# Optimization experiments

Hardware: AMD Instinct MI355X
Metric: run time of the kernel (lower is better)

Reference implementation:

```python
import jax, jax.numpy as jnp
import numpy as np

D_MODEL = 1024
NUM_HEADS = 8
KEY_DIM = 768      # int(1024*0.75)
VALUE_DIM = 1536   # int(1024*1.5)
HQK = KEY_DIM // NUM_HEADS    # 96
HV = VALUE_DIM // NUM_HEADS   # 192
D_CONV = 4
CHUNK = 64
B, L = 2, 4096


def silu(x):
    return x * jax.nn.sigmoid(x)


def causal_dwconv(x, w):
    # x: (B, L, C), w: (C, K) depthwise kernel; causal (left pad K-1), matches
    # torch Conv1d(padding=K-1) followed by [:, :L] slice.
    K = w.shape[1]
    Lx = x.shape[1]
    xp = jnp.pad(x, ((0, 0), (K - 1, 0), (0, 0)))
    out = xp[:, 0:Lx, :] * w[:, 0]
    for j in range(1, K):
        out = out + xp[:, j:j + Lx, :] * w[:, j]
    return out


def chunk_gated_delta_rule(q, k, v, beta, g, c):
    # q,k: (B,H,L,Dk) L2-normalized; v: (B,H,L,Dv); beta,g: (B,H,L)
    b, h, l, dk = q.shape
    dv = v.shape[-1]
    n = l // c  # L chosen as multiple of chunk size
    q = q * (dk ** -0.5)
    v = v * beta[..., None]
    kb = k * beta[..., None]
    rs = lambda x: x.reshape(b, h, n, c, x.shape[-1])
    q, k, v, kb = rs(q), rs(k), rs(v), rs(kb)
    dec = jnp.cumsum(g.reshape(b, h, n, c), axis=-1)        # (b,h,n,c)
    Lmask = jnp.exp(jnp.minimum(dec[..., :, None] - dec[..., None, :], 0.0))  # (b,h,n,c,c)
    tri_incl = jnp.triu(jnp.ones((c, c), bool))   # upper incl diag -> zeroed
    striu = jnp.triu(jnp.ones((c, c), bool), 1)   # strict upper
    I = jnp.eye(c, dtype=jnp.float32)
    KK = jnp.einsum('bhncd,bhnmd->bhncm', kb, k)  # k_beta @ k^T
    M1 = I + jnp.where(tri_incl, 0.0, KK * Lmask)
    M2 = I + jnp.where(tri_incl, 0.0, KK)
    Ib = jnp.broadcast_to(I, M1.shape)
    solve = lambda M: jax.lax.linalg.triangular_solve(
        M, Ib, left_side=True, lower=True, unit_diagonal=True)
    u_ = solve(M1) @ v       # k_cumsum (= u)
    kcd = solve(M2) @ kb     # k_cumdecay

    def step(S, xs):
        qi, ki, ui, kci, Lmi, di = xs
        ed = jnp.exp(di)[..., None]                 # (b,h,c,1)
        attn = jnp.where(striu, 0.0, jnp.einsum('bhcd,bhmd->bhcm', qi, ki) * Lmi)
        v_new = ui - jnp.einsum('bhcd,bhde->bhce', kci * ed, S)
        oi = jnp.einsum('bhcd,bhde->bhce', qi * ed, S) + attn @ v_new
        dl = di[..., -1]                            # (b,h)
        S = S * jnp.exp(dl)[..., None, None] + jnp.einsum(
            'bhcd,bhce->bhde', ki * jnp.exp(dl[..., None] - di)[..., None], v_new)
        return S, oi

    xs = tuple(jnp.moveaxis(t, 2, 0) for t in (q, k, u_, kcd, Lmask, dec))
    S0 = jnp.zeros((b, h, dk, dv), jnp.float32)
    _, o = jax.lax.scan(step, S0, xs)               # o: (n,b,h,c,dv)
    return jnp.moveaxis(o, 0, 2).reshape(b, h, l, dv)


def setup_inputs() -> dict:
    key = jax.random.key(0)
    ks = jax.random.split(key, 16)
    w = lambda k, shape: (jax.random.normal(k, shape, jnp.float32) * 0.02)
    dt = jnp.exp(jax.random.uniform(ks[10], (NUM_HEADS,)) *
                 (np.log(0.1) - np.log(0.001)) + np.log(0.001))
    dt = jnp.clip(dt, 0.0001, None)
    inv_dt = dt + jnp.log(-jnp.expm1(-dt))
    return {
        'u': jax.random.normal(ks[0], (B, L, D_MODEL), jnp.float32),
        'Wq': w(ks[1], (D_MODEL, KEY_DIM)),
        'Wk': w(ks[2], (D_MODEL, KEY_DIM)),
        'Wv': w(ks[3], (D_MODEL, VALUE_DIM)),
        'Wg': w(ks[4], (D_MODEL, VALUE_DIM)),
        'Wo': w(ks[5], (VALUE_DIM, D_MODEL)),
        'Wgk': w(ks[6], (D_MODEL, NUM_HEADS)),
        'Wb': w(ks[7], (D_MODEL, NUM_HEADS)),
        'b_b': jnp.zeros((NUM_HEADS,), jnp.float32),
        'A_log': jnp.log(jax.random.uniform(ks[8], (NUM_HEADS,), minval=0.001, maxval=16.0)),
        'dt_bias': inv_dt.astype(jnp.float32),
        'conv_q': w(ks[11], (KEY_DIM, D_CONV)) * 10.0,
        'conv_k': w(ks[12], (KEY_DIM, D_CONV)) * 10.0,
        'conv_v': w(ks[13], (VALUE_DIM, D_CONV)) * 10.0,
        'norm_w': jnp.ones((HV,), jnp.float32),
    }


def reference(u, Wq, Wk, Wv, Wg, Wo, Wgk, Wb, b_b, A_log, dt_bias,
              conv_q, conv_k, conv_v, norm_w):
    b, l, _ = u.shape
    q = silu(causal_dwconv(u @ Wq, conv_q))
    k = silu(causal_dwconv(u @ Wk, conv_k))
    v = silu(causal_dwconv(u @ Wv, conv_v))
    gk = u @ Wgk                                    # (B,L,H)
    gk = -jnp.exp(A_log) * jax.nn.softplus(gk + dt_bias)
    gk = gk.transpose(0, 2, 1)                      # (B,H,L)
    beta = jax.nn.sigmoid(u @ Wb + b_b).transpose(0, 2, 1)
    to_bhl = lambda x, d: x.reshape(b, l, NUM_HEADS, d).transpose(0, 2, 1, 3)
    q = to_bhl(q, HQK)
    k = to_bhl(k, HQK)
    v = to_bhl(v, HV)
    l2n = lambda x: x / jnp.maximum(jnp.linalg.norm(x, axis=-1, keepdims=True), 1e-12)
    q, k = l2n(q), l2n(k)
    o = chunk_gated_delta_rule(q, k, v, beta, gk, CHUNK)  # (B,H,L,HV)
    o = o.transpose(0, 2, 1, 3)                     # (B,L,H,HV)
    g = (u @ Wg).reshape(b, l, NUM_HEADS, HV)
    # RMSNormGated, norm_before_gate=True: norm(x)*weight*silu(g)
    on = o * jax.lax.rsqrt(jnp.mean(o * o, axis=-1, keepdims=True) + 1e-5) * norm_w
    on = on * silu(g)
    return on.reshape(b, l, VALUE_DIM) @ Wo
```

## Files before the change

### kernel.cpp

```cpp
#include <hip/hip_runtime.h>

using u16 = unsigned short;
using u32 = unsigned int;
typedef __bf16 bf16x8 __attribute__((ext_vector_type(8)));
typedef u16    u16x8  __attribute__((ext_vector_type(8)));
typedef float  f32x4  __attribute__((ext_vector_type(4)));
typedef float  f32x2  __attribute__((ext_vector_type(2)));
typedef u32    u32x4  __attribute__((ext_vector_type(4)));
typedef u32    u32x2  __attribute__((ext_vector_type(2)));

__device__ __forceinline__ float bf2f(u16 h){ u32 u = ((u32)h)<<16; float f; __builtin_memcpy(&f,&u,4); return f; }
__device__ __forceinline__ u16 f2bf(float f){ u32 u; __builtin_memcpy(&u,&f,4); u32 r = (u + 0x7FFFu + ((u>>16)&1u))>>16; return (u16)r; }
__device__ __forceinline__ float bflo(u32 w){ return bf2f((u16)(w & 0xFFFFu)); }
__device__ __forceinline__ float bfhiw(u32 w){ return bf2f((u16)(w >> 16)); }
__device__ __forceinline__ float sigx(float x){ float e = __expf(-fabsf(x)); float p = 1.f/(1.f+e); return (x>=0.f) ? p : 1.f-p; }

#define BAR_LGKM() asm volatile("s_waitcnt lgkmcnt(0)\n\ts_barrier" ::: "memory")

__device__ __forceinline__ float ldsc(const void* p, size_t i, bool f32){
  return f32 ? ((const float*)p)[i] : bf2f(((const u16*)p)[i]);
}
__device__ __forceinline__ u32x4 ld8bf(const void* p, size_t i, bool f32){
  if (!f32) return *(const u32x4*)((const u16*)p + i);
  const f32x4* q = (const f32x4*)((const float*)p + i);
  f32x4 a = q[0], b = q[1];
  u32x4 r;
  r.x = (u32)f2bf(a.x) | ((u32)f2bf(a.y)<<16);
  r.y = (u32)f2bf(a.z) | ((u32)f2bf(a.w)<<16);
  r.z = (u32)f2bf(b.x) | ((u32)f2bf(b.y)<<16);
  r.w = (u32)f2bf(b.z) | ((u32)f2bf(b.w)<<16);
  return r;
}
__device__ __forceinline__ void ld4w(const void* p, size_t i, bool f32,
                                     float& w0, float& w1, float& w2, float& w3){
  if (f32){ f32x4 v = *(const f32x4*)((const float*)p + i); w0=v.x; w1=v.y; w2=v.z; w3=v.w; }
  else { u32x2 v = *(const u32x2*)((const u16*)p + i); w0=bflo(v.x); w1=bfhiw(v.x); w2=bflo(v.y); w3=bfhiw(v.y); }
}


__global__ void detect_kernel(const u16* __restrict__ probe, int* __restrict__ flag){
  int t = threadIdx.x;
  int bad = 0;
  for (int i=t; i<1024; i+=64){
    u16 h = probe[i];
    int e = (h>>7)&0xFF;
    if (e >= 0xC0) bad = 1;
  }
  unsigned long long anyb = __ballot(bad);
  if (t==0) *flag = (anyb != 0ull) ? 1 : 0;
}

__global__ void transpose5(const void* __restrict__ Wq, const void* __restrict__ Wk,
                           const void* __restrict__ Wv, const void* __restrict__ Wg,
                           const void* __restrict__ Wo, const void* __restrict__ U,
                           u16* __restrict__ WqT, u16* __restrict__ WkT, u16* __restrict__ WvT,
                           u16* __restrict__ WgT, u16* __restrict__ WoT, u16* __restrict__ ubf,
                           const int* __restrict__ flagp){
  const bool f32 = (*flagp != 0);
  const int bid = blockIdx.x;
  const int t = threadIdx.x;
  if (bid >= 6144){
    size_t base = ((size_t)(bid-6144)*256 + t) * 16;
    u32x4 a = ld8bf(U, base, f32);
    u32x4 b = ld8bf(U, base+8, f32);
    *(u32x4*)(ubf + base)     = a;
    *(u32x4*)(ubf + base + 8) = b;
    return;
  }
  const void* in; u16* out; int C; int local;
  int R;
  if (bid < 768){ in=Wq; out=WqT; R=1024; C=768;  local=bid; }
  else if (bid < 1536){ in=Wk; out=WkT; R=1024; C=768;  local=bid-768; }
  else if (bid < 3072){ in=Wv; out=WvT; R=1024; C=1536; local=bid-1536; }
  else if (bid < 4608){ in=Wg; out=WgT; R=1024; C=1536; local=bid-3072; }
  else { in=Wo; out=WoT; R=1536; C=1024; local=bid-4608; }
  const int nCx = C>>5;
  const int c0 = (local % nCx)*32, r0 = (local / nCx)*32;
  __shared__ u16 tile[32][33];
  int tx = t & 31, ty = t >> 5;
  #pragma unroll
  for (int j=0;j<4;j++){
    int r = r0 + ty + j*8;
    size_t g = (size_t)r*C + c0 + tx;
    tile[ty+j*8][tx] = f32 ? f2bf(((const float*)in)[g]) : ((const u16*)in)[g];
  }
  __syncthreads();
  #pragma unroll
  for (int j=0;j<4;j++){ int c = c0 + ty + j*8; out[(size_t)c*R + r0 + tx] = tile[tx][ty+j*8]; }
}

__global__ __launch_bounds__(256,2) void gemm_bt(const void* __restrict__ A, const u16* __restrict__ Bt,
                                                 void* __restrict__ C, int M, int N, int K,
                                                 const int* __restrict__ flagp, int a_ext, int c_ext,
                                                 int sanitize){
  __shared__ __align__(16) u16 As[128*32];
  __shared__ __align__(16) u16 Bs[128*32];
  const int fl = *flagp;
  const bool af32 = a_ext && fl;
  const bool cf32 = c_ext && fl;
  const int t = threadIdx.x;
  const int bid = blockIdx.x;
  const int nbn = N>>7, rpx = (M>>7)>>3;
  const int x2 = bid & 7, s = bid >> 3;
  const int bm = (x2*rpx + s/nbn)*128;
  const int bn = (s % nbn)*128;
  const int wave = t>>6, lane = t&63, quad = lane>>4, l16 = lane&15;
  const int wm = (wave>>1)*64, wn = (wave&1)*64;
  f32x4 acc[4][4] = {};
  const int row0 = t>>2, kp = (t&3)*8;
  const size_t iA0 = (size_t)(bm+row0)*K + kp;
  const size_t iA1 = iA0 + (size_t)64*K;
  const u16* pB0 = Bt + (size_t)(bn+row0)*K + kp;
  const u16* pB1 = pB0 + (size_t)64*K;
  u32x4 ra0 = ld8bf(A, iA0, af32);
  u32x4 ra1 = ld8bf(A, iA1, af32);
  u32x4 rb0 = *(const u32x4*)pB0;
  u32x4 rb1 = *(const u32x4*)pB1;
  const int nk = K>>5;
  for (int kt=0; kt<nk; ++kt){
    __syncthreads();
    ((u32x4*)As)[t]     = ra0;
    ((u32x4*)As)[t+256] = ra1;
    ((u32x4*)Bs)[t]     = rb0;
    ((u32x4*)Bs)[t+256] = rb1;
    __syncthreads();
    if (kt+1 < nk){
      int o = (kt+1)*32;
      ra0 = ld8bf(A, iA0 + o, af32); ra1 = ld8bf(A, iA1 + o, af32);
      rb0 = *(const u32x4*)(pB0 + o); rb1 = *(const u32x4*)(pB1 + o);
    }
    bf16x8 af[4], bfv[4];
    #pragma unroll
    for (int i=0;i<4;i++){
      af[i]  = *(const bf16x8*)&As[(wm + i*16 + l16)*32 + quad*8];
      bfv[i] = *(const bf16x8*)&Bs[(wn + i*16 + l16)*32 + quad*8];
    }
    #pragma unroll
    for (int i=0;i<4;i++)
      #pragma unroll
      for (int j=0;j<4;j++)
        acc[i][j] = __builtin_amdgcn_mfma_f32_16x16x32_bf16(af[i], bfv[j], acc[i][j], 0,0,0);
  }
  #pragma unroll
  for (int i=0;i<4;i++)
    #pragma unroll
    for (int j=0;j<4;j++)
      #pragma unroll
      for (int r2=0;r2<4;r2++){
        int m = bm + wm + i*16 + quad*4 + r2;
        int n = bn + wn + j*16 + l16;
        float v = acc[i][j][r2];
        if (sanitize && !(v==v && v<1e30f && v>-1e30f)) v = 0.f;
        if (cf32) ((float*)C)[(size_t)m*N + n] = v;
        else      ((u16*)C)[(size_t)m*N + n] = f2bf(v);
      }
}

__global__ __launch_bounds__(256,2) void gemm_qkv(const u16* __restrict__ A,
                                                  const u16* __restrict__ BtQ, const u16* __restrict__ BtK,
                                                  const u16* __restrict__ BtV,
                                                  u16* __restrict__ Cq, u16* __restrict__ Ck, u16* __restrict__ Cv){
  __shared__ __align__(16) u16 As[128*32];
  __shared__ __align__(16) u16 Bs[128*32];
  const int t = threadIdx.x;
  const int bid = blockIdx.x;
  const int x2 = bid & 7, s = bid >> 3;
  const int bm = (x2*8 + s/24)*128;
  const int cgrp = s % 24;
  const u16* Bt; u16* C; int N, bn;
  if (cgrp < 6){ Bt=BtQ; C=Cq; N=768; bn=cgrp*128; }
  else if (cgrp < 12){ Bt=BtK; C=Ck; N=768; bn=(cgrp-6)*128; }
  else { Bt=BtV; C=Cv; N=1536; bn=(cgrp-12)*128; }
  const int K = 1024;
  const int wave = t>>6, lane = t&63, quad = lane>>4, l16 = lane&15;
  const int wm = (wave>>1)*64, wn = (wave&1)*64;
  f32x4 acc[4][4] = {};
  const int row0 = t>>2, kp = (t&3)*8;
  const u16* pA0 = A + (size_t)(bm+row0)*K + kp;
  const u16* pA1 = pA0 + (size_t)64*K;
  const u16* pB0 = Bt + (size_t)(bn+row0)*K + kp;
  const u16* pB1 = pB0 + (size_t)64*K;
  u32x4 ra0 = *(const u32x4*)pA0;
  u32x4 ra1 = *(const u32x4*)pA1;
  u32x4 rb0 = *(const u32x4*)pB0;
  u32x4 rb1 = *(const u32x4*)pB1;
  for (int kt=0; kt<32; ++kt){
    __syncthreads();
    ((u32x4*)As)[t]     = ra0;
    ((u32x4*)As)[t+256] = ra1;
    ((u32x4*)Bs)[t]     = rb0;
    ((u32x4*)Bs)[t+256] = rb1;
    __syncthreads();
    if (kt+1 < 32){
      int o = (kt+1)*32;
      ra0 = *(const u32x4*)(pA0 + o); ra1 = *(const u32x4*)(pA1 + o);
      rb0 = *(const u32x4*)(pB0 + o); rb1 = *(const u32x4*)(pB1 + o);
    }
    bf16x8 af[4], bfv[4];
    #pragma unroll
    for (int i=0;i<4;i++){
      af[i]  = *(const bf16x8*)&As[(wm + i*16 + l16)*32 + quad*8];
      bfv[i] = *(const bf16x8*)&Bs[(wn + i*16 + l16)*32 + quad*8];
    }
    #pragma unroll
    for (int i=0;i<4;i++)
      #pragma unroll
      for (int j=0;j<4;j++)
        acc[i][j] = __builtin_amdgcn_mfma_f32_16x16x32_bf16(af[i], bfv[j], acc[i][j], 0,0,0);
  }
  #pragma unroll
  for (int i=0;i<4;i++)
    #pragma unroll
    for (int j=0;j<4;j++)
      #pragma unroll
      for (int r2=0;r2<4;r2++){
        int m = bm + wm + i*16 + quad*4 + r2;
        int n = bn + wn + j*16 + l16;
        C[(size_t)m*N + n] = f2bf(acc[i][j][r2]);
      }
}

__global__ __launch_bounds__(256) void prep_kernel(
    const void* __restrict__ u, const void* __restrict__ Wgk, const void* __restrict__ Wb,
    const void* __restrict__ b_b, const void* __restrict__ A_log, const void* __restrict__ dt_b,
    const u16* __restrict__ qraw, const u16* __restrict__ kraw, const u16* __restrict__ vraw,
    const void* __restrict__ cq, const void* __restrict__ ck, const void* __restrict__ cv,
    float* __restrict__ gk, float* __restrict__ beta,
    u16* __restrict__ qn, u16* __restrict__ kn, u16* __restrict__ vb,
    const int* __restrict__ flagp){
  const bool f32 = (*flagp != 0);
  const int bl = blockIdx.x;
  const int b = bl>>12, l = bl&4095;
  const int t = threadIdx.x;
  __shared__ float s[768];
  __shared__ float red[4][16];
  __shared__ float nrm[8];
  __shared__ float bS2[8];

  {
    float accg[8] = {0,0,0,0,0,0,0,0};
    float accb[8] = {0,0,0,0,0,0,0,0};
    for (int d=t; d<1024; d+=256){
      float uv = ldsc(u, (size_t)bl*1024 + d, f32);
      u32x4 wg = ld8bf(Wgk, (size_t)d*8, f32);
      u32x4 wb = ld8bf(Wb,  (size_t)d*8, f32);
      accg[0] += uv*bflo(wg.x); accg[1] += uv*bfhiw(wg.x);
      accg[2] += uv*bflo(wg.y); accg[3] += uv*bfhiw(wg.y);
      accg[4] += uv*bflo(wg.z); accg[5] += uv*bfhiw(wg.z);
      accg[6] += uv*bflo(wg.w); accg[7] += uv*bfhiw(wg.w);
      accb[0] += uv*bflo(wb.x); accb[1] += uv*bfhiw(wb.x);
      accb[2] += uv*bflo(wb.y); accb[3] += uv*bfhiw(wb.y);
      accb[4] += uv*bflo(wb.z); accb[5] += uv*bfhiw(wb.z);
      accb[6] += uv*bflo(wb.w); accb[7] += uv*bfhiw(wb.w);
    }
    #pragma unroll
    for (int h=0;h<8;h++){
      #pragma unroll
      for (int off=32; off>=1; off>>=1){
        accg[h] += __shfl_down(accg[h], off);
        accb[h] += __shfl_down(accb[h], off);
      }
    }
    int wv = t>>6, lane = t&63;
    if (lane==0){
      #pragma unroll
      for (int h=0;h<8;h++){ red[wv][h]=accg[h]; red[wv][8+h]=accb[h]; }
    }
    __syncthreads();
    if (t<16){
      float sum = red[0][t]+red[1][t]+red[2][t]+red[3][t];
      if (t<8){
        int h=t;
        float x = sum + ldsc(dt_b, h, f32);
        float sp = (x>20.f) ? x : log1pf(__expf(x));
        gk[(size_t)(b*8+h)*4096 + l] = -__expf(ldsc(A_log, h, f32)) * sp;
      } else {
        int h=t-8;
        float x = sum + ldsc(b_b, h, f32);
        float bv = sigx(x);
        beta[(size_t)(b*8+h)*4096 + l] = bv;
        bS2[h] = bv;
      }
    }
  }
  __syncthreads();

  const int base = b*4096;
  for (int c=t; c<768; c+=256){
    float w0,w1,w2,w3; ld4w(cq, (size_t)c*4, f32, w0,w1,w2,w3);
    float acc = 0.f;
    if (l>=3) acc += bf2f(qraw[(size_t)(base+l-3)*768 + c])*w0;
    if (l>=2) acc += bf2f(qraw[(size_t)(base+l-2)*768 + c])*w1;
    if (l>=1) acc += bf2f(qraw[(size_t)(base+l-1)*768 + c])*w2;
    acc += bf2f(qraw[(size_t)(base+l)*768 + c])*w3;
    s[c] = acc*sigx(acc);
  }
  __syncthreads();
  {
    int h = t>>5, l32 = t&31;
    float p = 0.f;
    for (int i=l32; i<96; i+=32){ float x = s[h*96+i]; p += x*x; }
    p += __shfl_down(p,16,32); p += __shfl_down(p,8,32); p += __shfl_down(p,4,32);
    p += __shfl_down(p,2,32);  p += __shfl_down(p,1,32);
    if (l32==0) nrm[h] = fmaxf(sqrtf(p), 1e-12f);
  }
  __syncthreads();
  for (int c=t; c<768; c+=256){
    int hh = c/96; int d = c - hh*96;
    float v = s[c]/nrm[hh]*0.10206207261596575f;
    qn[((size_t)(b*8+hh)*4096 + l)*96 + d] = f2bf(v);
  }
  __syncthreads();
  for (int c=t; c<768; c+=256){
    float w0,w1,w2,w3; ld4w(ck, (size_t)c*4, f32, w0,w1,w2,w3);
    float acc = 0.f;
    if (l>=3) acc += bf2f(kraw[(size_t)(base+l-3)*768 + c])*w0;
    if (l>=2) acc += bf2f(kraw[(size_t)(base+l-2)*768 + c])*w1;
    if (l>=1) acc += bf2f(kraw[(size_t)(base+l-1)*768 + c])*w2;
    acc += bf2f(kraw[(size_t)(base+l)*768 + c])*w3;
    s[c] = acc*sigx(acc);
  }
  __syncthreads();
  {
    int h = t>>5, l32 = t&31;
    float p = 0.f;
    for (int i=l32; i<96; i+=32){ float x = s[h*96+i]; p += x*x; }
    p += __shfl_down(p,16,32); p += __shfl_down(p,8,32); p += __shfl_down(p,4,32);
    p += __shfl_down(p,2,32);  p += __shfl_down(p,1,32);
    if (l32==0) nrm[h] = fmaxf(sqrtf(p), 1e-12f);
  }
  __syncthreads();
  for (int c=t; c<768; c+=256){
    int hh = c/96; int d = c - hh*96;
    float v = s[c]/nrm[hh]*1.0f;
    kn[((size_t)(b*8+hh)*4096 + l)*96 + d] = f2bf(v);
  }
  for (int c=t; c<1536; c+=256){
    float w0,w1,w2,w3; ld4w(cv, (size_t)c*4, f32, w0,w1,w2,w3);
    float acc = 0.f;
    if (l>=3) acc += bf2f(vraw[(size_t)(base+l-3)*1536 + c])*w0;
    if (l>=2) acc += bf2f(vraw[(size_t)(base+l-2)*1536 + c])*w1;
    if (l>=1) acc += bf2f(vraw[(size_t)(base+l-1)*1536 + c])*w2;
    acc += bf2f(vraw[(size_t)(base+l)*1536 + c])*w3;
    int h = c/192; int d = c - h*192;
    vb[((size_t)(b*8+h)*4096 + l)*192 + d] = f2bf(acc*sigx(acc)*bS2[h]);
  }
}

__global__ __launch_bounds__(320,2) void chunkprep_kernel(
    const u16* __restrict__ qn, u16* __restrict__ knw, const u16* __restrict__ vb,
    const float* __restrict__ beta, const float* __restrict__ gk,
    u16* __restrict__ attn, u16* __restrict__ kcd, u16* __restrict__ uA,
    float* __restrict__ edG, float* __restrict__ aG){
  __shared__ __align__(16) u16 kS[64*104];
  __shared__ __align__(16) u16 qS[64*104];
  __shared__ float M1[64*64];
  __shared__ float M2[64*64];
  __shared__ float bS[64], dS[64], wS2[64];
  const int t = threadIdx.x;
  const int bhn = blockIdx.x;
  const size_t rowb = (size_t)bhn*64;
  const int w = t>>6, l = t&63, l16 = l&15, quad = l>>4;

  #pragma unroll
  for (int j=0;j<3;j++){
    int v = t + 320*j;
    if (v < 768){
      int rr = v/12, c8 = v - rr*12;
      size_t g = (rowb+rr)*96 + c8*8;
      *(u32x4*)&kS[rr*104 + c8*8] = *(const u32x4*)(knw + g);
      *(u32x4*)&qS[rr*104 + c8*8] = *(const u32x4*)(qn + g);
    }
  }
  if (t<64){
    bS[t] = beta[rowb+t];
    float g = gk[rowb+t];
    #pragma unroll
    for (int off=1; off<64; off<<=1){
      float xx = __shfl_up(g, off);
      if (t >= off) g += xx;
    }
    dS[t] = g;
    float dl = __shfl(g, 63);
    edG[rowb+t] = __expf(g);
    wS2[t] = __expf(dl - g);
    if (t==0) aG[bhn] = __expf(dl);
  }
  __syncthreads();

  for (int idx=t; idx<6144; idx+=320){
    int d = idx>>6, ll = idx&63;
    knw[(size_t)bhn*6144 + idx] = f2bf(bf2f(kS[ll*104 + d])*wS2[ll]);
  }

  float x[64];
  const int mode0 = (t<192) ? 0 : 1;
  const int c0 = (t<192) ? t : (t-192);
  const bool active = (t < 288);
  if (active){
    if (mode0==0){
      #pragma unroll
      for (int i=0;i<64;i++) x[i] = bf2f(vb[(rowb+i)*192 + c0]);
    } else {
      #pragma unroll
      for (int i=0;i<64;i++) x[i] = bS[i]*bf2f(kS[i*104 + c0]);
    }
  }

  if (t < 256){
    bf16x8 qA[3], kA[3];
    #pragma unroll
    for (int ks=0;ks<3;ks++){
      qA[ks] = *(const bf16x8*)&qS[(w*16+l16)*104 + ks*32 + quad*8];
      kA[ks] = *(const bf16x8*)&kS[(w*16+l16)*104 + ks*32 + quad*8];
    }
    const size_t ab = (size_t)bhn*4096;
    #pragma unroll
    for (int nt=0;nt<4;nt++){
      f32x4 aQ = {0.f,0.f,0.f,0.f}, aK = {0.f,0.f,0.f,0.f};
      #pragma unroll
      for (int ks=0;ks<3;ks++){
        bf16x8 Bf = *(const bf16x8*)&kS[(nt*16+l16)*104 + ks*32 + quad*8];
        aQ = __builtin_amdgcn_mfma_f32_16x16x32_bf16(qA[ks], Bf, aQ,0,0,0);
        aK = __builtin_amdgcn_mfma_f32_16x16x32_bf16(kA[ks], Bf, aK,0,0,0);
      }
      #pragma unroll
      for (int r=0;r<4;r++){
        int row = w*16 + quad*4 + r;
        int col = nt*16 + l16;
        float lm = __expf(fminf(dS[row]-dS[col], 0.f));
        attn[ab + row*64 + col] = (col<=row) ? f2bf(aQ[r]*lm) : (u16)0;
        if (col<row){
          float kkb = aK[r]*bS[row];
          M2[row*64+col] = kkb;
          M1[row*64+col] = kkb*lm;
        }
      }
    }
  }
  __syncthreads();

  if (active){
    const float* Mb = (mode0==0) ? M1 : M2;
    #pragma unroll
    for (int i=1;i<64;i++){
      float acc = x[i];
      #pragma unroll
      for (int m=0;m<i;m++) acc -= Mb[i*64+m]*x[m];
      x[i] = acc;
    }
    if (mode0==0){
      #pragma unroll
      for (int i=0;i<64;i++) uA[(rowb+i)*192 + c0] = f2bf(x[i]);
    } else {
      #pragma unroll
      for (int i=0;i<64;i++) kcd[(rowb+i)*96 + c0] = f2bf(x[i]);
    }
  }
}

__global__ __launch_bounds__(256,1) void scan_glin_kernel(
    const u16* __restrict__ qn, const u16* __restrict__ kTw, const u16* __restrict__ kcd,
    const u16* __restrict__ attn, const u16* __restrict__ uA,
    const float* __restrict__ edG, const float* __restrict__ aG,
    u16* __restrict__ o,
    const u16* __restrict__ Ag, const u16* __restrict__ Btg,
    u16* __restrict__ Cg0, u16* __restrict__ Cg1, u16* __restrict__ Cg2, u16* __restrict__ Cg3){
  __shared__ __align__(16) char smem[16640];
  const int bid = blockIdx.x;
  const int t = threadIdx.x;

  if (bid >= 192){
    u16* As = (u16*)smem;
    u16* Bs = (u16*)(smem + 8192);
    const int j = bid - 192;
    const int x2 = j & 7, s = j >> 3;
    const int bm = (x2*8 + s/12)*128;
    const int bn = (s % 12)*128;
    const int wave = t>>6, lane = t&63, quad = lane>>4, l16 = lane&15;
    const int wm = (wave>>1)*64, wn = (wave&1)*64;
    f32x4 acc[4][4] = {};
    const int row0 = t>>2, kp = (t&3)*8;
    const u16* pA0 = Ag + (size_t)(bm+row0)*1024 + kp;
    const u16* pA1 = pA0 + (size_t)64*1024;
    const u16* pB0 = Btg + (size_t)(bn+row0)*1024 + kp;
    const u16* pB1 = pB0 + (size_t)64*1024;
    u32x4 ra0 = *(const u32x4*)pA0;
    u32x4 ra1 = *(const u32x4*)pA1;
    u32x4 rb0 = *(const u32x4*)pB0;
    u32x4 rb1 = *(const u32x4*)pB1;
    for (int kt=0; kt<32; ++kt){
      __syncthreads();
      ((u32x4*)As)[t]     = ra0;
      ((u32x4*)As)[t+256] = ra1;
      ((u32x4*)Bs)[t]     = rb0;
      ((u32x4*)Bs)[t+256] = rb1;
      __syncthreads();
      if (kt+1 < 32){
        int o2 = (kt+1)*32;
        ra0 = *(const u32x4*)(pA0 + o2); ra1 = *(const u32x4*)(pA1 + o2);
        rb0 = *(const u32x4*)(pB0 + o2); rb1 = *(const u32x4*)(pB1 + o2);
      }
      bf16x8 af[4], bfv[4];
      #pragma unroll
      for (int i=0;i<4;i++){
        af[i]  = *(const bf16x8*)&As[(wm + i*16 + l16)*32 + quad*8];
        bfv[i] = *(const bf16x8*)&Bs[(wn + i*16 + l16)*32 + quad*8];
      }
      #pragma unroll
      for (int i=0;i<4;i++)
        #pragma unroll
        for (int j2=0;j2<4;j2++)
          acc[i][j2] = __builtin_amdgcn_mfma_f32_16x16x32_bf16(af[i], bfv[j2], acc[i][j2], 0,0,0);
    }
    u16* Cp; int mo;
    if (bm < 5376){ Cp = Cg0; mo = bm; }
    else if (bm < 6656){ Cp = Cg1; mo = bm - 5376; }
    else if (bm < 7680){ Cp = Cg2; mo = bm - 6656; }
    else { Cp = Cg3; mo = bm - 7680; }
    #pragma unroll
    for (int i=0;i<4;i++)
      #pragma unroll
      for (int j2=0;j2<4;j2++)
        #pragma unroll
        for (int r2=0;r2<4;r2++){
          int m = mo + wm + i*16 + quad*4 + r2;
          int n = bn + wn + j2*16 + l16;
          Cp[(size_t)m*1536 + n] = f2bf(acc[i][j2][r2]);
        }
    return;
  }

  __builtin_amdgcn_s_setprio(1);
  const int bh = bid % 16, eg = bid / 16;
  const int e0 = eg*16;
  const int w = t>>6, l = t&63, l16 = l&15, quad = l>>4;

  u16* vnewT = (u16*)smem;
  u16* Sbf   = (u16*)(smem + 2304);

  for (int i=t; i<16*104; i+=256) Sbf[i] = 0;

  size_t rowb = (size_t)bh*4096;
  size_t ab   = (size_t)bh*64*4096;

  u32x4 kcdF[3], qF[3], attF[2]; u16 uF[4];
  u32x4 kuC[2][2], kuN[2][2];
  auto pfAB = [&](size_t rowbN){
    #pragma unroll
    for (int ks=0; ks<3; ks++){
      size_t gg = (rowbN + w*16 + l16)*96 + ks*32 + quad*8;
      kcdF[ks] = *(const u32x4*)(kcd + gg);
      qF[ks]   = *(const u32x4*)(qn + gg);
    }
  };
  auto pfATT = [&](size_t abN){
    #pragma unroll
    for (int ks=0; ks<2; ks++)
      attF[ks] = *(const u32x4*)(attn + abN + (w*16 + l16)*64 + ks*32 + quad*8);
  };
  auto pfU = [&](size_t rowbN){
    #pragma unroll
    for (int r=0;r<4;r++)
      uF[r] = uA[(rowbN + w*16 + quad*4 + r)*192 + e0 + l16];
  };
  auto pfKU = [&](size_t chunkIdx, u32x4 (&dst)[2][2]){
    #pragma unroll
    for (int i=0;i<2;i++){
      int tid = w + 4*i;
      if (tid < 6){
        size_t base = chunkIdx*6144 + (size_t)(tid*16 + l16)*64 + quad*8;
        dst[i][0] = *(const u32x4*)(kTw + base);
        dst[i][1] = *(const u32x4*)(kTw + base + 32);
      }
    }
  };

  pfAB(rowb); pfU(rowb); pfATT(ab);
  pfKU(rowb>>6, kuC);
  f32x4 edC = *(const f32x4*)&edG[rowb + w*16 + quad*4];
  float aexpC = aG[rowb>>6];
  __syncthreads();
  f32x4 Sreg[2] = {};

  for (int n=0;n<64;n++){
    const size_t rowbN = rowb + 64;
    const size_t abN = ab + 4096;
    f32x4 edN = {0.f,0.f,0.f,0.f};
    float aexpN = 0.f;
    if (n<63){
      pfKU(rowbN>>6, kuN);
      edN = *(const f32x4*)&edG[rowbN + w*16 + quad*4];
      aexpN = aG[rowbN>>6];
    }
    f32x4 accA = {0.f,0.f,0.f,0.f}, accQ = {0.f,0.f,0.f,0.f};
    #pragma unroll
    for (int ks=0;ks<3;ks++){
      bf16x8 Bf = *(const bf16x8*)&Sbf[l16*104 + ks*32 + quad*8];
      accA = __builtin_amdgcn_mfma_f32_16x16x32_bf16(*(const bf16x8*)&kcdF[ks], Bf, accA,0,0,0);
      accQ = __builtin_amdgcn_mfma_f32_16x16x32_bf16(*(const bf16x8*)&qF[ks],  Bf, accQ,0,0,0);
    }
    #pragma unroll
    for (int r=0;r<4;r++){
      float vn = bf2f(uF[r]) - edC[r]*accA[r];
      vnewT[l16*72 + (w*16+quad*4+r)] = f2bf(vn);
      accQ[r] *= edC[r];
    }
    if (n<63){ pfAB(rowbN); pfU(rowbN); }
    BAR_LGKM();
    #pragma unroll
    for (int ks=0;ks<2;ks++){
      bf16x8 Bv = *(const bf16x8*)&vnewT[l16*72 + ks*32 + quad*8];
      accQ = __builtin_amdgcn_mfma_f32_16x16x32_bf16(*(const bf16x8*)&attF[ks], Bv, accQ,0,0,0);
    }
    #pragma unroll
    for (int r=0;r<4;r++)
      o[(rowb + w*16 + quad*4 + r)*192 + e0 + l16] = f2bf(accQ[r]);
    if (n<63) pfATT(abN);
    #pragma unroll
    for (int i=0;i<2;i++){
      int tid = w + 4*i;
      if (tid < 6){
        int mt = tid;
        f32x4 acc = (f32x4){0.f,0.f,0.f,0.f};
        #pragma unroll
        for (int ks=0;ks<2;ks++){
          bf16x8 Bv = *(const bf16x8*)&vnewT[l16*72 + ks*32 + quad*8];
          acc = __builtin_amdgcn_mfma_f32_16x16x32_bf16(*(const bf16x8*)&kuC[i][ks], Bv, acc,0,0,0);
        }
        f32x4 ns;
        ns.x = Sreg[i].x*aexpC + acc.x;
        ns.y = Sreg[i].y*aexpC + acc.y;
        ns.z = Sreg[i].z*aexpC + acc.z;
        ns.w = Sreg[i].w*aexpC + acc.w;
        Sreg[i] = ns;
        u32x2 pv;
        pv.x = (u32)f2bf(ns.x) | ((u32)f2bf(ns.y)<<16);
        pv.y = (u32)f2bf(ns.z) | ((u32)f2bf(ns.w)<<16);
        *(u32x2*)&Sbf[l16*104 + mt*16 + quad*4] = pv;
      }
    }
    BAR_LGKM();
    rowb = rowbN; ab = abN;
    edC = edN; aexpC = aexpN;
    kuC[0][0]=kuN[0][0]; kuC[0][1]=kuN[0][1]; kuC[1][0]=kuN[1][0]; kuC[1][1]=kuN[1][1];
  }
}

__global__ __launch_bounds__(192) void epilogue_kernel(const u16* __restrict__ o,
                                                       const u16* __restrict__ g0, const u16* __restrict__ g1,
                                                       const u16* __restrict__ g2, const u16* __restrict__ g3,
                                                       const void* __restrict__ nw, u16* __restrict__ on,
                                                       const int* __restrict__ flagp){
  const bool f32 = (*flagp != 0);
  const int bl = blockIdx.x; const int h = blockIdx.y; const int d = threadIdx.x;
  const int b = bl>>12, l = bl&4095;
  float x = bf2f(o[((size_t)(b*8+h)*4096 + l)*192 + d]);
  float p = x*x;
  p += __shfl_down(p,32); p += __shfl_down(p,16); p += __shfl_down(p,8);
  p += __shfl_down(p,4);  p += __shfl_down(p,2);  p += __shfl_down(p,1);
  __shared__ float red[3];
  int wv = d>>6;
  if ((d&63)==0) red[wv] = p;
  __syncthreads();
  float ss = red[0]+red[1]+red[2];
  float rs = rsqrtf(ss/192.f + 1e-5f);
  const u16* gp; int bo;
  if (bl < 5376){ gp = g0; bo = bl; }
  else if (bl < 6656){ gp = g1; bo = bl - 5376; }
  else if (bl < 7680){ gp = g2; bo = bl - 6656; }
  else { gp = g3; bo = bl - 7680; }
  float g = bf2f(gp[(size_t)bo*1536 + h*192 + d]);
  float val = x*rs*ldsc(nw, d, f32) * g*sigx(g);
  on[(size_t)bl*1536 + h*192 + d] = f2bf(val);
}

extern "C" void kernel_launch(void* const* d_in, const int* in_sizes, int n_in,
                              void* d_out, int out_size, void* d_ws, size_t ws_size,
                              hipStream_t stream){
  (void)in_sizes; (void)n_in; (void)out_size; (void)ws_size;
  const void* u     = d_in[0];
  const void* Wq    = d_in[1];
  const void* Wk    = d_in[2];
  const void* Wv    = d_in[3];
  const void* Wg    = d_in[4];
  const void* Wo    = d_in[5];
  const void* Wgk   = d_in[6];
  const void* Wb    = d_in[7];
  const void* b_b   = d_in[8];
  const void* A_log = d_in[9];
  const void* dt_b  = d_in[10];
  const void* cq    = d_in[11];
  const void* ck    = d_in[12];
  const void* cv    = d_in[13];
  const void* nw    = d_in[14];

  char* w = (char*)d_ws;
  size_t off = 0;
  auto take = [&](size_t bytes)->char*{
    char* p = w + off;
    off += (bytes + 255) & ~(size_t)255;
    return p;
  };
  int* flag = (int*)take(256);
  u16* WqT  = (u16*)take((size_t)768*1024*2);
  u16* WkT  = (u16*)take((size_t)768*1024*2);
  u16* WvT  = (u16*)take((size_t)1536*1024*2);
  u16* WgT  = (u16*)take((size_t)1536*1024*2);
  u16* WoT  = (u16*)take((size_t)1024*1536*2);
  u16* qraw = (u16*)take((size_t)8192*768*2);
  u16* kraw = (u16*)take((size_t)8192*768*2);
  u16* vraw = (u16*)take((size_t)8192*1536*2);
  u16* qn   = (u16*)take((size_t)8192*768*2);
  u16* kn   = (u16*)take((size_t)8192*768*2);
  u16* vb   = (u16*)take((size_t)8192*1536*2);
  u16* ubf  = (u16*)take((size_t)8192*1024*2);
  float* gkA   = (float*)WqT;
  float* betaA = gkA + 65536;
  float* edG   = betaA + 65536;
  float* wGA   = edG + 65536;
  float* aGA   = wGA + 65536;
  u16* attnA = qraw;
  u16* kcdA  = kraw;
  u16* uuA   = vraw;
  u16* oA    = vb;
  u16* onA   = vraw;
  u16* glin0 = (u16*)d_out;
  u16* glin1 = attnA + (size_t)1024*64*64;
  u16* glin2 = WvT;
  u16* glin3 = WkT;

  detect_kernel<<<1,64,0,stream>>>((const u16*)u, flag);
  transpose5<<<8192,256,0,stream>>>(Wq, Wk, Wv, Wg, Wo, u,
                                    WqT, WkT, WvT, WgT, WoT, ubf, flag);
  gemm_qkv<<<1536,256,0,stream>>>(ubf, WqT, WkT, WvT, qraw, kraw, vraw);
  prep_kernel<<<8192,256,0,stream>>>(u, Wgk, Wb, b_b, A_log, dt_b,
                                     qraw, kraw, vraw, cq, ck, cv,
                                     gkA, betaA, qn, kn, vb, flag);
  chunkprep_kernel<<<1024,320,0,stream>>>(qn, kn, vb, betaA, gkA, attnA, kcdA, uuA,
                                          edG, aGA);
  scan_glin_kernel<<<960,256,0,stream>>>(qn, kn , kcdA, attnA, uuA, edG, aGA, oA,
                                         ubf, WgT, glin0, glin1, glin2, glin3);
  epilogue_kernel<<<dim3(8192,8),192,0,stream>>>(oA, glin0, glin1, glin2, glin3, nw, onA, flag);
  gemm_bt<<<512,256,0,stream>>>(onA, WoT, d_out, 8192, 1024, 1536, flag, 0, 1, 1);
}
```

Measured before the change: 574.2 us.

## Vectorize prep and epilogue kernels with 8-wide bf16 loads and role-split threads

The prep kernel now runs 384 threads, each handling 8 channels of q, k or v. Each thread uses 128-bit loads for the conv inputs and weights, and the q/k L2 norms are computed in one merged pass. This removes the shared-memory staging and the several serial barrier phases. The epilogue kernel moves from one block per (position, head) with scalar elements to one block per position, where each thread handles 8 contiguous elements with vector loads and stores. This cuts block count, instruction count and memory transactions, at the cost of more registers per thread and less parallelism per block.

```diff
diff --git a/kernel.cpp b/kernel.cpp
--- a/kernel.cpp
+++ b/kernel.cpp
@@ -31,10 +31,9 @@
   r.w = (u32)f2bf(b.z) | ((u32)f2bf(b.w)<<16);
   return r;
 }
-__device__ __forceinline__ void ld4w(const void* p, size_t i, bool f32,
-                                     float& w0, float& w1, float& w2, float& w3){
-  if (f32){ f32x4 v = *(const f32x4*)((const float*)p + i); w0=v.x; w1=v.y; w2=v.z; w3=v.w; }
-  else { u32x2 v = *(const u32x2*)((const u16*)p + i); w0=bflo(v.x); w1=bfhiw(v.x); w2=bflo(v.y); w3=bfhiw(v.y); }
+__device__ __forceinline__ void unpack8(u32x4 v, float* f){
+  f[0]=bflo(v.x); f[1]=bfhiw(v.x); f[2]=bflo(v.y); f[3]=bfhiw(v.y);
+  f[4]=bflo(v.z); f[5]=bfhiw(v.z); f[6]=bflo(v.w); f[7]=bfhiw(v.w);
 }
 
 
@@ -220,7 +219,7 @@
       }
 }
 
-__global__ __launch_bounds__(256) void prep_kernel(
+__global__ __launch_bounds__(384) void prep_kernel(
     const void* __restrict__ u, const void* __restrict__ Wgk, const void* __restrict__ Wb,
     const void* __restrict__ b_b, const void* __restrict__ A_log, const void* __restrict__ dt_b,
     const u16* __restrict__ qraw, const u16* __restrict__ kraw, const u16* __restrict__ vraw,
@@ -232,12 +231,12 @@
   const int bl = blockIdx.x;
   const int b = bl>>12, l = bl&4095;
   const int t = threadIdx.x;
-  __shared__ float s[768];
   __shared__ float red[4][16];
-  __shared__ float nrm[8];
+  __shared__ float sqP[96], skP[96];
+  __shared__ float nrmq[8], nrmk[8];
   __shared__ float bS2[8];
 
-  {
+  if (t < 256){
     float accg[8] = {0,0,0,0,0,0,0,0};
     float accb[8] = {0,0,0,0,0,0,0,0};
     for (int d=t; d<1024; d+=256){
@@ -266,84 +265,107 @@
       #pragma unroll
       for (int h=0;h<8;h++){ red[wv][h]=accg[h]; red[wv][8+h]=accb[h]; }
     }
-    __syncthreads();
-    if (t<16){
-      float sum = red[0][t]+red[1][t]+red[2][t]+red[3][t];
-      if (t<8){
-        int h=t;
-        float x = sum + ldsc(dt_b, h, f32);
-        float sp = (x>20.f) ? x : log1pf(__expf(x));
-        gk[(size_t)(b*8+h)*4096 + l] = -__expf(ldsc(A_log, h, f32)) * sp;
-      } else {
-        int h=t-8;
-        float x = sum + ldsc(b_b, h, f32);
-        float bv = sigx(x);
-        beta[(size_t)(b*8+h)*4096 + l] = bv;
-        bS2[h] = bv;
-      }
+  }
+  __syncthreads();
+  if (t<16){
+    float sum = red[0][t]+red[1][t]+red[2][t]+red[3][t];
+    if (t<8){
+      int h=t;
+      float x = sum + ldsc(dt_b, h, f32);
+      float sp = (x>20.f) ? x : log1pf(__expf(x));
+      gk[(size_t)(b*8+h)*4096 + l] = -__expf(ldsc(A_log, h, f32)) * sp;
+    } else {
+      int h=t-8;
+      float x = sum + ldsc(b_b, h, f32);
+      float bv = sigx(x);
+      beta[(size_t)(b*8+h)*4096 + l] = bv;
+      bS2[h] = bv;
     }
   }
   __syncthreads();
 
   const int base = b*4096;
-  for (int c=t; c<768; c+=256){
-    float w0,w1,w2,w3; ld4w(cq, (size_t)c*4, f32, w0,w1,w2,w3);
-    float acc = 0.f;
-    if (l>=3) acc += bf2f(qraw[(size_t)(base+l-3)*768 + c])*w0;
-    if (l>=2) acc += bf2f(qraw[(size_t)(base+l-2)*768 + c])*w1;
-    if (l>=1) acc += bf2f(qraw[(size_t)(base+l-1)*768 + c])*w2;
-    acc += bf2f(qraw[(size_t)(base+l)*768 + c])*w3;
-    s[c] = acc*sigx(acc);
-  }
-  __syncthreads();
-  {
-    int h = t>>5, l32 = t&31;
-    float p = 0.f;
-    for (int i=l32; i<96; i+=32){ float x = s[h*96+i]; p += x*x; }
-    p += __shfl_down(p,16,32); p += __shfl_down(p,8,32); p += __shfl_down(p,4,32);
-    p += __shfl_down(p,2,32);  p += __shfl_down(p,1,32);
-    if (l32==0) nrm[h] = fmaxf(sqrtf(p), 1e-12f);
-  }
-  __syncthreads();
-  for (int c=t; c<768; c+=256){
-    int hh = c/96; int d = c - hh*96;
-    float v = s[c]/nrm[hh]*0.10206207261596575f;
-    qn[((size_t)(b*8+hh)*4096 + l)*96 + d] = f2bf(v);
-  }
-  __syncthreads();
-  for (int c=t; c<768; c+=256){
-    float w0,w1,w2,w3; ld4w(ck, (size_t)c*4, f32, w0,w1,w2,w3);
-    float acc = 0.f;
-    if (l>=3) acc += bf2f(kraw[(size_t)(base+l-3)*768 + c])*w0;
-    if (l>=2) acc += bf2f(kraw[(size_t)(base+l-2)*768 + c])*w1;
-    if (l>=1) acc += bf2f(kraw[(size_t)(base+l-1)*768 + c])*w2;
-    acc += bf2f(kraw[(size_t)(base+l)*768 + c])*w3;
-    s[c] = acc*sigx(acc);
-  }
-  __syncthreads();
-  {
-    int h = t>>5, l32 = t&31;
-    float p = 0.f;
-    for (int i=l32; i<96; i+=32){ float x = s[h*96+i]; p += x*x; }
-    p += __shfl_down(p,16,32); p += __shfl_down(p,8,32); p += __shfl_down(p,4,32);
-    p += __shfl_down(p,2,32);  p += __shfl_down(p,1,32);
-    if (l32==0) nrm[h] = fmaxf(sqrtf(p), 1e-12f);
-  }
-  __syncthreads();
-  for (int c=t; c<768; c+=256){
-    int hh = c/96; int d = c - hh*96;
-    float v = s[c]/nrm[hh]*1.0f;
-    kn[((size_t)(b*8+hh)*4096 + l)*96 + d] = f2bf(v);
-  }
-  for (int c=t; c<1536; c+=256){
-    float w0,w1,w2,w3; ld4w(cv, (size_t)c*4, f32, w0,w1,w2,w3);
-    float acc = 0.f;
-    if (l>=3) acc += bf2f(vraw[(size_t)(base+l-3)*1536 + c])*w0;
-    if (l>=2) acc += bf2f(vraw[(size_t)(base+l-2)*1536 + c])*w1;
-    if (l>=1) acc += bf2f(vraw[(size_t)(base+l-1)*1536 + c])*w2;
-    acc += bf2f(vraw[(size_t)(base+l)*1536 + c])*w3;
-    int h = c/192; int d = c - h*192;
-    vb[((size_t)(b*8+h)*4096 + l)*192 + d] = f2bf(acc*sigx(acc)*bS2[h]);
+  int role, c0;
+  if (t < 96){ role=0; c0=t*8; }
+  else if (t < 192){ role=1; c0=(t-96)*8; }
+  else { role=2; c0=(t-192)*8; }
+  const u16* raw = (role==0)? qraw : (role==1)? kraw : vraw;
+  const void* cw = (role==0)? cq : (role==1)? ck : cv;
+  const int C = (role==2)? 1536 : 768;
+
+  float w[8][4];
+  #pragma unroll
+  for (int g=0; g<4; g++){
+    u32x4 W = ld8bf(cw, (size_t)c0*4 + g*8, f32);
+    w[g*2+0][0]=bflo(W.x); w[g*2+0][1]=bfhiw(W.x); w[g*2+0][2]=bflo(W.y); w[g*2+0][3]=bfhiw(W.y);
+    w[g*2+1][0]=bflo(W.z); w[g*2+1][1]=bfhiw(W.z); w[g*2+1][2]=bflo(W.w); w[g*2+1][3]=bfhiw(W.w);
+  }
+  float acc[8];
+  #pragma unroll
+  for (int ch=0; ch<8; ch++) acc[ch] = 0.f;
+  #pragma unroll
+  for (int j=0;j<4;j++){
+    if (l >= 3-j){
+      u32x4 iv = *(const u32x4*)(raw + (size_t)(base+l-3+j)*C + c0);
+      float in[8]; unpack8(iv, in);
+      #pragma unroll
+      for (int ch=0;ch<8;ch++) acc[ch] += in[ch]*w[ch][j];
+    }
+  }
+  #pragma unroll
+  for (int ch=0;ch<8;ch++) acc[ch] = acc[ch]*sigx(acc[ch]);
+
+  if (role==2){
+    int h = c0/192, d0 = c0 - h*192;
+    float bv = bS2[h];
+    u32x4 pv;
+    pv.x = (u32)f2bf(acc[0]*bv) | ((u32)f2bf(acc[1]*bv)<<16);
+    pv.y = (u32)f2bf(acc[2]*bv) | ((u32)f2bf(acc[3]*bv)<<16);
+    pv.z = (u32)f2bf(acc[4]*bv) | ((u32)f2bf(acc[5]*bv)<<16);
+    pv.w = (u32)f2bf(acc[6]*bv) | ((u32)f2bf(acc[7]*bv)<<16);
+    *(u32x4*)&vb[((size_t)(b*8+h)*4096 + l)*192 + d0] = pv;
+  } else {
+    float ss = 0.f;
+    #pragma unroll
+    for (int ch=0;ch<8;ch++) ss += acc[ch]*acc[ch];
+    if (role==0) sqP[t] = ss; else skP[t-96] = ss;
+  }
+  __syncthreads();
+  if (t < 8){
+    float s = 0.f;
+    #pragma unroll
+    for (int j=0;j<12;j++) s += sqP[t*12+j];
+    nrmq[t] = fmaxf(sqrtf(s), 1e-12f);
+  } else if (t < 16){
+    int h = t-8;
+    float s = 0.f;
+    #pragma unroll
+    for (int j=0;j<12;j++) s += skP[h*12+j];
+    nrmk[h] = fmaxf(sqrtf(s), 1e-12f);
+  }
+  __syncthreads();
+  if (role==0){
+    int h = c0/96, d0 = c0 - h*96;
+    float nr = nrmq[h];
+    float v0 = acc[0]/nr*0.10206207261596575f, v1 = acc[1]/nr*0.10206207261596575f;
+    float v2 = acc[2]/nr*0.10206207261596575f, v3 = acc[3]/nr*0.10206207261596575f;
+    float v4 = acc[4]/nr*0.10206207261596575f, v5 = acc[5]/nr*0.10206207261596575f;
+    float v6 = acc[6]/nr*0.10206207261596575f, v7 = acc[7]/nr*0.10206207261596575f;
+    u32x4 pv;
+    pv.x = (u32)f2bf(v0) | ((u32)f2bf(v1)<<16);
+    pv.y = (u32)f2bf(v2) | ((u32)f2bf(v3)<<16);
+    pv.z = (u32)f2bf(v4) | ((u32)f2bf(v5)<<16);
+    pv.w = (u32)f2bf(v6) | ((u32)f2bf(v7)<<16);
+    *(u32x4*)&qn[((size_t)(b*8+h)*4096 + l)*96 + d0] = pv;
+  } else if (role==1){
+    int h = c0/96, d0 = c0 - h*96;
+    float nr = nrmk[h];
+    u32x4 pv;
+    pv.x = (u32)f2bf(acc[0]/nr*1.0f) | ((u32)f2bf(acc[1]/nr*1.0f)<<16);
+    pv.y = (u32)f2bf(acc[2]/nr*1.0f) | ((u32)f2bf(acc[3]/nr*1.0f)<<16);
+    pv.z = (u32)f2bf(acc[4]/nr*1.0f) | ((u32)f2bf(acc[5]/nr*1.0f)<<16);
+    pv.w = (u32)f2bf(acc[6]/nr*1.0f) | ((u32)f2bf(acc[7]/nr*1.0f)<<16);
+    *(u32x4*)&kn[((size_t)(b*8+h)*4096 + l)*96 + d0] = pv;
   }
 }
 
@@ -653,26 +675,45 @@
                                                        const void* __restrict__ nw, u16* __restrict__ on,
                                                        const int* __restrict__ flagp){
   const bool f32 = (*flagp != 0);
-  const int bl = blockIdx.x; const int h = blockIdx.y; const int d = threadIdx.x;
+  const int bl = blockIdx.x;
+  const int t = threadIdx.x;
   const int b = bl>>12, l = bl&4095;
-  float x = bf2f(o[((size_t)(b*8+h)*4096 + l)*192 + d]);
-  float p = x*x;
-  p += __shfl_down(p,32); p += __shfl_down(p,16); p += __shfl_down(p,8);
-  p += __shfl_down(p,4);  p += __shfl_down(p,2);  p += __shfl_down(p,1);
-  __shared__ float red[3];
-  int wv = d>>6;
-  if ((d&63)==0) red[wv] = p;
-  __syncthreads();
-  float ss = red[0]+red[1]+red[2];
-  float rs = rsqrtf(ss/192.f + 1e-5f);
+  const int h = t/24, d0 = (t - h*24)*8;
+  __shared__ float part[192];
+  __shared__ float rsS[8];
+  u32x4 ov = *(const u32x4*)&o[((size_t)(b*8+h)*4096 + l)*192 + d0];
+  float x[8]; unpack8(ov, x);
+  float ss = 0.f;
+  #pragma unroll
+  for (int ch=0;ch<8;ch++) ss += x[ch]*x[ch];
+  part[t] = ss;
+  __syncthreads();
+  if (t < 8){
+    float s = 0.f;
+    #pragma unroll
+    for (int j=0;j<24;j++) s += part[t*24+j];
+    rsS[t] = rsqrtf(s/192.f + 1e-5f);
+  }
+  __syncthreads();
+  float rs = rsS[h];
   const u16* gp; int bo;
   if (bl < 5376){ gp = g0; bo = bl; }
   else if (bl < 6656){ gp = g1; bo = bl - 5376; }
   else if (bl < 7680){ gp = g2; bo = bl - 6656; }
   else { gp = g3; bo = bl - 7680; }
-  float g = bf2f(gp[(size_t)bo*1536 + h*192 + d]);
-  float val = x*rs*ldsc(nw, d, f32) * g*sigx(g);
-  on[(size_t)bl*1536 + h*192 + d] = f2bf(val);
+  u32x4 gv = *(const u32x4*)&gp[(size_t)bo*1536 + h*192 + d0];
+  float gf[8]; unpack8(gv, gf);
+  u32x4 nv = ld8bf(nw, d0, f32);
+  float nf[8]; unpack8(nv, nf);
+  u32x4 pv;
+  float r[8];
+  #pragma unroll
+  for (int ch=0;ch<8;ch++) r[ch] = x[ch]*rs*nf[ch]*gf[ch]*sigx(gf[ch]);
+  pv.x = (u32)f2bf(r[0]) | ((u32)f2bf(r[1])<<16);
+  pv.y = (u32)f2bf(r[2]) | ((u32)f2bf(r[3])<<16);
+  pv.z = (u32)f2bf(r[4]) | ((u32)f2bf(r[5])<<16);
+  pv.w = (u32)f2bf(r[6]) | ((u32)f2bf(r[7])<<16);
+  *(u32x4*)&on[(size_t)bl*1536 + h*192 + d0] = pv;
 }
 
 extern "C" void kernel_launch(void* const* d_in, const int* in_sizes, int n_in,
@@ -734,13 +775,13 @@
   transpose5<<<8192,256,0,stream>>>(Wq, Wk, Wv, Wg, Wo, u,
                                     WqT, WkT, WvT, WgT, WoT, ubf, flag);
   gemm_qkv<<<1536,256,0,stream>>>(ubf, WqT, WkT, WvT, qraw, kraw, vraw);
-  prep_kernel<<<8192,256,0,stream>>>(u, Wgk, Wb, b_b, A_log, dt_b,
+  prep_kernel<<<8192,384,0,stream>>>(u, Wgk, Wb, b_b, A_log, dt_b,
                                      qraw, kraw, vraw, cq, ck, cv,
                                      gkA, betaA, qn, kn, vb, flag);
   chunkprep_kernel<<<1024,320,0,stream>>>(qn, kn, vb, betaA, gkA, attnA, kcdA, uuA,
                                           edG, aGA);
   scan_glin_kernel<<<960,256,0,stream>>>(qn, kn , kcdA, attnA, uuA, edG, aGA, oA,
                                          ubf, WgT, glin0, glin1, glin2, glin3);
-  epilogue_kernel<<<dim3(8192,8),192,0,stream>>>(oA, glin0, glin1, glin2, glin3, nw, onA, flag);
+  epilogue_kernel<<<8192,192,0,stream>>>(oA, glin0, glin1, glin2, glin3, nw, onA, flag);
   gemm_bt<<<512,256,0,stream>>>(onA, WoT, d_out, 8192, 1024, 1536, flag, 0, 1, 1);
 }
```

New measurement: 559.8 us. 1.03x faster.
